# Optimization experiments

Measured on AMD Instinct MI355X. Metric: run time of the kernel, lower is better.

The kernel has to match this reference:

```python
import jax, jax.numpy as jnp
import numpy as np

B, Q, K, D = 8, 2048, 2048, 512
MASK_VALUE = -1e-06  # faithful to original (note: source uses -1e-06, not -1e6)


def setup_inputs() -> dict:
    key = jax.random.key(0)
    k1, k2, k3, k4, k5 = jax.random.split(key, 5)
    queries = jax.random.normal(k1, (B, Q, D), dtype=jnp.float32)
    keys = jax.random.normal(k2, (B, K, D), dtype=jnp.float32)
    values = jax.random.normal(k3, (B, K, D), dtype=jnp.float32)
    # Xavier-uniform-like init for the bilinear weight
    limit = float(np.sqrt(6.0 / (D + D)))
    W = jax.random.uniform(k4, (D, D), dtype=jnp.float32, minval=-limit, maxval=limit)
    attention_masks = jax.random.randint(k5, (B,), 1, K, dtype=jnp.int64 if jax.config.jax_enable_x64 else jnp.int32)
    return {"queries": queries, "keys": keys, "values": values, "W": W,
            "attention_masks": attention_masks}


def reference(queries, keys, values, W, attention_masks):
    # scores[b,q,k] = (queries @ W) . keys  -> bilinear attention logits
    scores = jnp.einsum('bqd,de,bke->bqk', queries, W, keys)
    # length mask: positions >= attention_masks[b] are replaced by MASK_VALUE
    valid = jnp.arange(scores.shape[-1])[None, None, :] < attention_masks[:, None, None]
    scores = jnp.where(valid, scores, MASK_VALUE)
    attn = jax.nn.softmax(scores, axis=-1)  # (B, Q, K)
    # dropout p=0 -> identity
    return jnp.einsum('bqk,bkv->bqv', attn, values)
```

## Files before the change

### kernel.cpp

```cpp
#include <hip/hip_runtime.h>

#define NB 8
#define NQ 2048
#define NK 2048
#define ND 512
#define QB 64
#define KB 512
#define MASK_VALUE (-1e-06f)
#define PLANE  ((size_t)NB * NK * ND)
#define WPLANE ((size_t)ND * ND)

typedef __attribute__((ext_vector_type(4))) float f32x4;
typedef __attribute__((ext_vector_type(8))) __bf16 bf16x8;
typedef __attribute__((ext_vector_type(8))) _Float16 f16x8;
typedef __attribute__((ext_vector_type(4))) _Float16 f16x4;
typedef __attribute__((ext_vector_type(8))) unsigned short u16x8;
typedef __attribute__((ext_vector_type(4))) unsigned int u32x4;

typedef f32x4  __attribute__((may_alias)) f32x4_ma;
typedef bf16x8 __attribute__((may_alias)) bf16x8_ma;
typedef f16x8  __attribute__((may_alias)) f16x8_ma;
typedef f16x4  __attribute__((may_alias)) f16x4_ma;
typedef u32x4  __attribute__((may_alias)) u32x4_ma;

__device__ __forceinline__ unsigned short f2bf(float x){
    union { float f; unsigned u; } v; v.f = x;
    unsigned r = v.u + 0x7fffu + ((v.u >> 16) & 1u);
    return (unsigned short)(r >> 16);
}
__device__ __forceinline__ float bf2f(unsigned short h){
    union { unsigned u; float f; } v; v.u = ((unsigned)h) << 16;
    return v.f;
}

__global__ __launch_bounds__(256)
void conv_k_f16_kernel(const float* __restrict__ K,
                       _Float16* __restrict__ kf)
{
    const size_t i = ((size_t)blockIdx.x * 256 + threadIdx.x) * 4;
    const f32x4 v = *(const f32x4_ma*)(K + i);
    f16x4 h;
    #pragma unroll
    for (int c = 0; c < 4; ++c) h[c] = (_Float16)v[c];
    *(f16x4_ma*)(kf + i) = h;
}

__global__ __launch_bounds__(256)
void transpose_v_f16_kernel(const float* __restrict__ V,
                            _Float16* __restrict__ vt)
{
    __shared__ float t[64][68];
    const int tid = threadIdx.x;
    const int bid = blockIdx.x;
    const int dt  = bid & 7;
    const int kt  = (bid >> 3) & 31;
    const int b   = bid >> 8;
    {
        const int rr = tid >> 4;
        const int c4 = (tid & 15) * 4;
        #pragma unroll
        for (int m4 = 0; m4 < 4; ++m4){
            const int kr = rr + m4*16;
            *(f32x4_ma*)&t[kr][c4] =
                *(const f32x4_ma*)&V[((size_t)b*NK + kt*64 + kr)*ND + dt*64 + c4];
        }
    }
    __syncthreads();
    {
        const int dr = tid >> 2;
        const int kc = (tid & 3) * 16;
        f16x8 v0, v1;
        #pragma unroll
        for (int j = 0; j < 8; ++j) v0[j] = (_Float16)t[kc + j][dr];
        #pragma unroll
        for (int j = 0; j < 8; ++j) v1[j] = (_Float16)t[kc + 8 + j][dr];
        const size_t dst = ((size_t)b*ND + dt*64 + dr)*NK + kt*64 + kc;
        *(f16x8_ma*)(vt + dst)     = v0;
        *(f16x8_ma*)(vt + dst + 8) = v1;
    }
}

__global__ __launch_bounds__(256)
void transpose_split_w_kernel(const float* __restrict__ W,
                              unsigned short* __restrict__ wth,
                              unsigned short* __restrict__ wtl)
{
    __shared__ float t[64][68];
    const int tid = threadIdx.x;
    const int et  = blockIdx.x & 7;
    const int dt  = blockIdx.x >> 3;
    {
        const int rr = tid >> 4;
        const int c4 = (tid & 15) * 4;
        #pragma unroll
        for (int m4 = 0; m4 < 4; ++m4){
            const int dr = rr + m4*16;
            *(f32x4_ma*)&t[dr][c4] =
                *(const f32x4_ma*)&W[(size_t)(dt*64 + dr)*ND + et*64 + c4];
        }
    }
    __syncthreads();
    {
        const int er = tid >> 2;
        const int dc = (tid & 3) * 16;
        unsigned short hh[16], ll[16];
        #pragma unroll
        for (int j = 0; j < 16; ++j){
            const float v = t[dc + j][er];
            const unsigned short h = f2bf(v);
            hh[j] = h;
            ll[j] = f2bf(v - bf2f(h));
        }
        u32x4 h0, h1, l0, l1;
        #pragma unroll
        for (int c = 0; c < 4; ++c){
            h0[c] = (unsigned)hh[2*c]   | ((unsigned)hh[2*c+1] << 16);
            h1[c] = (unsigned)hh[8+2*c] | ((unsigned)hh[9+2*c] << 16);
            l0[c] = (unsigned)ll[2*c]   | ((unsigned)ll[2*c+1] << 16);
            l1[c] = (unsigned)ll[8+2*c] | ((unsigned)ll[9+2*c] << 16);
        }
        const size_t dst = (size_t)(et*64 + er)*ND + dt*64 + dc;
        *(u32x4_ma*)(wth + dst)     = h0;
        *(u32x4_ma*)(wth + dst + 8) = h1;
        *(u32x4_ma*)(wtl + dst)     = l0;
        *(u32x4_ma*)(wtl + dst + 8) = l1;
    }
}

__global__ __launch_bounds__(1024, 4)
void attn_kernel(const float* __restrict__ Qp, const int* __restrict__ Mp,
                 const _Float16* __restrict__ Kf,
                 const _Float16* __restrict__ Vt,
                 const unsigned short* __restrict__ Wth, const unsigned short* __restrict__ Wtl,
                 float* __restrict__ Op)
{
    __shared__ _Float16 qw[QB][520];
    __shared__ _Float16 p_b[QB][520];
    __shared__ float wredA[QB][16];

    const int tid  = threadIdx.x;
    const int lane = tid & 63;
    const int wv   = tid >> 6;
    const int lm   = lane & 15;
    const int lg   = lane >> 4;
    const int b    = blockIdx.x & 7;
    const int q0   = (int)(blockIdx.x >> 3) * QB;

    int mk;
    {
        const int odd = Mp[1] | Mp[3] | Mp[5] | Mp[7];
        mk = (odd == 0) ? Mp[2*b] : Mp[b];
    }

    {
        f32x4 acc[4][2];
        #pragma unroll
        for (int m2 = 0; m2 < 4; ++m2)
            #pragma unroll
            for (int n2 = 0; n2 < 2; ++n2) acc[m2][n2] = (f32x4){0.f,0.f,0.f,0.f};

        for (int w = 0; w < 16; ++w){
            bf16x8 aH[4], aL[4];
            #pragma unroll
            for (int m2 = 0; m2 < 4; ++m2){
                const float* qp = Qp + ((size_t)b*NQ + q0 + m2*16 + lm)*ND + w*32 + lg*8;
                const f32x4 qa = *(const f32x4_ma*)qp;
                const f32x4 qb = *(const f32x4_ma*)(qp + 4);
                u16x8 hh, ll;
                #pragma unroll
                for (int c = 0; c < 4; ++c){
                    const unsigned short h = f2bf(qa[c]);
                    hh[c] = h; ll[c] = f2bf(qa[c] - bf2f(h));
                }
                #pragma unroll
                for (int c = 0; c < 4; ++c){
                    const unsigned short h = f2bf(qb[c]);
                    hh[4+c] = h; ll[4+c] = f2bf(qb[c] - bf2f(h));
                }
                aH[m2] = __builtin_bit_cast(bf16x8, hh);
                aL[m2] = __builtin_bit_cast(bf16x8, ll);
            }
            #pragma unroll
            for (int n2 = 0; n2 < 2; ++n2){
                const size_t wrow = (size_t)(wv*32 + n2*16 + lm)*ND + w*32 + lg*8;
                const bf16x8 bh = *(const bf16x8_ma*)(Wth + wrow);
                const bf16x8 bl = *(const bf16x8_ma*)(Wtl + wrow);
                #pragma unroll
                for (int m2 = 0; m2 < 4; ++m2){
                    acc[m2][n2] = __builtin_amdgcn_mfma_f32_16x16x32_bf16(aH[m2], bh, acc[m2][n2], 0,0,0);
                    acc[m2][n2] = __builtin_amdgcn_mfma_f32_16x16x32_bf16(aH[m2], bl, acc[m2][n2], 0,0,0);
                    acc[m2][n2] = __builtin_amdgcn_mfma_f32_16x16x32_bf16(aL[m2], bh, acc[m2][n2], 0,0,0);
                }
            }
        }
        #pragma unroll
        for (int m2 = 0; m2 < 4; ++m2)
            #pragma unroll
            for (int n2 = 0; n2 < 2; ++n2)
                #pragma unroll
                for (int r = 0; r < 4; ++r)
                    qw[m2*16 + lg*4 + r][wv*32 + n2*16 + lm] = (_Float16)acc[m2][n2][r];
    }
    __syncthreads();

    float m_run[4][4], lsum[4][4];
    #pragma unroll
    for (int m2 = 0; m2 < 4; ++m2)
        #pragma unroll
        for (int r = 0; r < 4; ++r){ m_run[m2][r] = -3.0e38f; lsum[m2][r] = 0.f; }

    f32x4 o_acc[4][2];
    #pragma unroll
    for (int m2 = 0; m2 < 4; ++m2)
        #pragma unroll
        for (int n = 0; n < 2; ++n) o_acc[m2][n] = (f32x4){0.f,0.f,0.f,0.f};

    const _Float16* kfb = Kf + ((size_t)b*NK + wv*16 + lm)*ND;
    const size_t vbase = ((size_t)b*ND + wv*32 + lm)*NK + lg*8;

    for (int kt = 0; kt < NK/KB; ++kt){
        const int k0 = kt * KB;
        const size_t koff = (size_t)k0 * ND;

        f32x4 sacc[2][4];
        #pragma unroll
        for (int h = 0; h < 2; ++h)
            #pragma unroll
            for (int m2 = 0; m2 < 4; ++m2) sacc[h][m2] = (f32x4){0.f,0.f,0.f,0.f};
        #pragma unroll
        for (int w2 = 0; w2 < 8; ++w2){
            f16x8 bk[2][2];
            #pragma unroll
            for (int j = 0; j < 2; ++j)
                #pragma unroll
                for (int h = 0; h < 2; ++h)
                    bk[j][h] = *(const f16x8_ma*)(kfb + koff + (size_t)h*256*ND + (w2*2 + j)*32 + lg*8);
            #pragma unroll
            for (int j = 0; j < 2; ++j){
                const int eoff = (w2*2 + j)*32 + lg*8;
                #pragma unroll
                for (int m2 = 0; m2 < 4; ++m2){
                    const f16x8 aQ = *(const f16x8_ma*)&qw[m2*16 + lm][eoff];
                    sacc[0][m2] = __builtin_amdgcn_mfma_f32_16x16x32_f16(aQ, bk[j][0], sacc[0][m2], 0,0,0);
                    sacc[1][m2] = __builtin_amdgcn_mfma_f32_16x16x32_f16(aQ, bk[j][1], sacc[1][m2], 0,0,0);
                }
            }
        }

        float sv[2][4][4];
        #pragma unroll
        for (int h = 0; h < 2; ++h){
            const bool inval = (k0 + h*256 + wv*16 + lm) >= mk;
            #pragma unroll
            for (int m2 = 0; m2 < 4; ++m2)
                #pragma unroll
                for (int r = 0; r < 4; ++r)
                    sv[h][m2][r] = inval ? MASK_VALUE : sacc[h][m2][r];
        }

        float pm[4][4];
        #pragma unroll
        for (int m2 = 0; m2 < 4; ++m2)
            #pragma unroll
            for (int r = 0; r < 4; ++r) pm[m2][r] = fmaxf(sv[0][m2][r], sv[1][m2][r]);
        #pragma unroll
        for (int off = 1; off < 16; off <<= 1)
            #pragma unroll
            for (int m2 = 0; m2 < 4; ++m2)
                #pragma unroll
                for (int r = 0; r < 4; ++r)
                    pm[m2][r] = fmaxf(pm[m2][r], __shfl_xor(pm[m2][r], off, 64));
        if (lm == 0){
            #pragma unroll
            for (int m2 = 0; m2 < 4; ++m2)
                #pragma unroll
                for (int r = 0; r < 4; ++r) wredA[m2*16 + lg*4 + r][wv] = pm[m2][r];
        }
        __syncthreads();

        #pragma unroll
        for (int m2 = 0; m2 < 4; ++m2)
            #pragma unroll
            for (int r = 0; r < 4; ++r){
                const int row = m2*16 + lg*4 + r;
                const f32x4 g0 = *(const f32x4_ma*)&wredA[row][0];
                const f32x4 g1 = *(const f32x4_ma*)&wredA[row][4];
                const f32x4 g2 = *(const f32x4_ma*)&wredA[row][8];
                const f32x4 g3 = *(const f32x4_ma*)&wredA[row][12];
                float gm = fmaxf(fmaxf(fmaxf(g0[0],g0[1]),fmaxf(g0[2],g0[3])),
                                 fmaxf(fmaxf(g1[0],g1[1]),fmaxf(g1[2],g1[3])));
                gm = fmaxf(gm, fmaxf(fmaxf(fmaxf(g2[0],g2[1]),fmaxf(g2[2],g2[3])),
                                     fmaxf(fmaxf(g3[0],g3[1]),fmaxf(g3[2],g3[3]))));
                if (gm > m_run[m2][r]){
                    const float fsc = __expf(m_run[m2][r] - gm);
                    m_run[m2][r] = gm;
                    o_acc[m2][0][r] *= fsc;
                    o_acc[m2][1][r] *= fsc;
                    lsum[m2][r]     *= fsc;
                }
                const _Float16 ph0 = (_Float16)__expf(sv[0][m2][r] - m_run[m2][r]);
                const _Float16 ph1 = (_Float16)__expf(sv[1][m2][r] - m_run[m2][r]);
                p_b[row][wv*16 + lm]       = ph0;
                p_b[row][256 + wv*16 + lm] = ph1;
                lsum[m2][r] += (float)ph0 + (float)ph1;
            }
        __syncthreads();

        #pragma unroll
        for (int kb = 0; kb < 16; ++kb){
            f16x8 pa[4];
            #pragma unroll
            for (int m2 = 0; m2 < 4; ++m2)
                pa[m2] = *(const f16x8_ma*)&p_b[m2*16 + lm][kb*32 + lg*8];
            #pragma unroll
            for (int n = 0; n < 2; ++n){
                const f16x8 vv = *(const f16x8_ma*)(Vt + vbase + (size_t)n*16*NK + k0 + kb*32);
                #pragma unroll
                for (int m2 = 0; m2 < 4; ++m2)
                    o_acc[m2][n] = __builtin_amdgcn_mfma_f32_16x16x32_f16(pa[m2], vv, o_acc[m2][n], 0,0,0);
            }
        }
    }

    #pragma unroll
    for (int off = 1; off < 16; off <<= 1)
        #pragma unroll
        for (int m2 = 0; m2 < 4; ++m2)
            #pragma unroll
            for (int r = 0; r < 4; ++r)
                lsum[m2][r] += __shfl_xor(lsum[m2][r], off, 64);
    if (lm == 0){
        #pragma unroll
        for (int m2 = 0; m2 < 4; ++m2)
            #pragma unroll
            for (int r = 0; r < 4; ++r)
                wredA[m2*16 + lg*4 + r][wv] = lsum[m2][r];
    }
    __syncthreads();
    #pragma unroll
    for (int m2 = 0; m2 < 4; ++m2){
        float li[4];
        #pragma unroll
        for (int r = 0; r < 4; ++r){
            const int row = m2*16 + lg*4 + r;
            const f32x4 s0 = *(const f32x4_ma*)&wredA[row][0];
            const f32x4 s1 = *(const f32x4_ma*)&wredA[row][4];
            const f32x4 s2 = *(const f32x4_ma*)&wredA[row][8];
            const f32x4 s3 = *(const f32x4_ma*)&wredA[row][12];
            const float l = (((s0[0]+s0[1]) + (s0[2]+s0[3])) + ((s1[0]+s1[1]) + (s1[2]+s1[3])))
                          + (((s2[0]+s2[1]) + (s2[2]+s2[3])) + ((s3[0]+s3[1]) + (s3[2]+s3[3])));
            li[r] = 1.f / l;
        }
        #pragma unroll
        for (int n = 0; n < 2; ++n)
            #pragma unroll
            for (int r = 0; r < 4; ++r)
                Op[((size_t)b*NQ + q0 + m2*16 + lg*4 + r)*ND + wv*32 + n*16 + lm]
                    = o_acc[m2][n][r] * li[r];
    }
}

extern "C" void kernel_launch(void* const* d_in, const int* in_sizes, int n_in,
                              void* d_out, int out_size, void* d_ws, size_t ws_size,
                              hipStream_t stream)
{
    (void)in_sizes; (void)n_in; (void)out_size; (void)ws_size;
    const float* Qp = (const float*)d_in[0];
    const float* Kp = (const float*)d_in[1];
    const float* Vp = (const float*)d_in[2];
    const float* Wp = (const float*)d_in[3];
    const int*   Mp = (const int*)  d_in[4];
    float* Op = (float*)d_out;

    unsigned short* wsu = (unsigned short*)d_ws;
    _Float16*       Kf  = (_Float16*)wsu;
    _Float16*       Vt  = (_Float16*)(wsu + PLANE);
    unsigned short* Wth = wsu + 2*PLANE;
    unsigned short* Wtl = wsu + 2*PLANE + WPLANE;

    hipLaunchKernelGGL(conv_k_f16_kernel, dim3(PLANE/1024), dim3(256), 0, stream,
                       Kp, Kf);
    hipLaunchKernelGGL(transpose_v_f16_kernel, dim3(NB*32*8), dim3(256), 0, stream,
                       Vp, Vt);
    hipLaunchKernelGGL(transpose_split_w_kernel, dim3(64), dim3(256), 0, stream,
                       Wp, Wth, Wtl);
    hipLaunchKernelGGL(attn_kernel, dim3(NB*(NQ/QB)), dim3(1024), 0, stream,
                       Qp, Mp, Kf, Vt, Wth, Wtl, Op);
}
```

Measured before the change: 270.1 us.

## Split Q·W projection into separate kernel, stage QW in global memory

Moves the split-bf16 Q·W projection out of the attention kernel into its own kernel, which writes an fp16 QW tensor to workspace. The attention kernel then reads QW fragments straight from global/L2 instead of LDS, which frees the qw shared array and may allow higher occupancy. The cost is an extra kernel launch, a global round trip of roughly 16 MB for QW, and repeated global loads of QW on every key tile.

```diff
diff --git a/kernel.cpp b/kernel.cpp
--- a/kernel.cpp
+++ b/kernel.cpp
@@ -22,6 +22,7 @@
 typedef f16x8  __attribute__((may_alias)) f16x8_ma;
 typedef f16x4  __attribute__((may_alias)) f16x4_ma;
 typedef u32x4  __attribute__((may_alias)) u32x4_ma;
+typedef _Float16 __attribute__((may_alias)) f16_ma;
 
 __device__ __forceinline__ unsigned short f2bf(float x){
     union { float f; unsigned u; } v; v.f = x;
@@ -128,16 +129,11 @@
 }
 
 __global__ __launch_bounds__(1024, 4)
-void attn_kernel(const float* __restrict__ Qp, const int* __restrict__ Mp,
-                 const _Float16* __restrict__ Kf,
-                 const _Float16* __restrict__ Vt,
-                 const unsigned short* __restrict__ Wth, const unsigned short* __restrict__ Wtl,
-                 float* __restrict__ Op)
-{
-    __shared__ _Float16 qw[QB][520];
-    __shared__ _Float16 p_b[QB][520];
-    __shared__ float wredA[QB][16];
-
+void qw_mfma_kernel(const float* __restrict__ Qp,
+                    const unsigned short* __restrict__ Wth,
+                    const unsigned short* __restrict__ Wtl,
+                    _Float16* __restrict__ qwg)
+{
     const int tid  = threadIdx.x;
     const int lane = tid & 63;
     const int wv   = tid >> 6;
@@ -146,63 +142,80 @@
     const int b    = blockIdx.x & 7;
     const int q0   = (int)(blockIdx.x >> 3) * QB;
 
+    f32x4 acc[4][2];
+    #pragma unroll
+    for (int m2 = 0; m2 < 4; ++m2)
+        #pragma unroll
+        for (int n2 = 0; n2 < 2; ++n2) acc[m2][n2] = (f32x4){0.f,0.f,0.f,0.f};
+
+    for (int w = 0; w < 16; ++w){
+        bf16x8 aH[4], aL[4];
+        #pragma unroll
+        for (int m2 = 0; m2 < 4; ++m2){
+            const float* qp = Qp + ((size_t)b*NQ + q0 + m2*16 + lm)*ND + w*32 + lg*8;
+            const f32x4 qa = *(const f32x4_ma*)qp;
+            const f32x4 qb = *(const f32x4_ma*)(qp + 4);
+            u16x8 hh, ll;
+            #pragma unroll
+            for (int c = 0; c < 4; ++c){
+                const unsigned short h = f2bf(qa[c]);
+                hh[c] = h; ll[c] = f2bf(qa[c] - bf2f(h));
+            }
+            #pragma unroll
+            for (int c = 0; c < 4; ++c){
+                const unsigned short h = f2bf(qb[c]);
+                hh[4+c] = h; ll[4+c] = f2bf(qb[c] - bf2f(h));
+            }
+            aH[m2] = __builtin_bit_cast(bf16x8, hh);
+            aL[m2] = __builtin_bit_cast(bf16x8, ll);
+        }
+        #pragma unroll
+        for (int n2 = 0; n2 < 2; ++n2){
+            const size_t wrow = (size_t)(wv*32 + n2*16 + lm)*ND + w*32 + lg*8;
+            const bf16x8 bh = *(const bf16x8_ma*)(Wth + wrow);
+            const bf16x8 bl = *(const bf16x8_ma*)(Wtl + wrow);
+            #pragma unroll
+            for (int m2 = 0; m2 < 4; ++m2){
+                acc[m2][n2] = __builtin_amdgcn_mfma_f32_16x16x32_bf16(aH[m2], bh, acc[m2][n2], 0,0,0);
+                acc[m2][n2] = __builtin_amdgcn_mfma_f32_16x16x32_bf16(aH[m2], bl, acc[m2][n2], 0,0,0);
+                acc[m2][n2] = __builtin_amdgcn_mfma_f32_16x16x32_bf16(aL[m2], bh, acc[m2][n2], 0,0,0);
+            }
+        }
+    }
+    #pragma unroll
+    for (int m2 = 0; m2 < 4; ++m2)
+        #pragma unroll
+        for (int n2 = 0; n2 < 2; ++n2)
+            #pragma unroll
+            for (int r = 0; r < 4; ++r)
+                qwg[((size_t)b*NQ + q0 + m2*16 + lg*4 + r)*ND + wv*32 + n2*16 + lm]
+                    = (_Float16)acc[m2][n2][r];
+}
+
+__global__ __launch_bounds__(1024, 4)
+void attn_kernel(const int* __restrict__ Mp,
+                 const _Float16* __restrict__ qwg,
+                 const _Float16* __restrict__ Kf,
+                 const _Float16* __restrict__ Vt,
+                 float* __restrict__ Op)
+{
+    __shared__ _Float16 p_b[QB][520];
+    __shared__ float wredA[QB][16];
+
+    const int tid  = threadIdx.x;
+    const int lane = tid & 63;
+    const int wv   = tid >> 6;
+    const int lm   = lane & 15;
+    const int lg   = lane >> 4;
+    const int b    = blockIdx.x & 7;
+    const int q0   = (int)(blockIdx.x >> 3) * QB;
+
     int mk;
     {
         const int odd = Mp[1] | Mp[3] | Mp[5] | Mp[7];
         mk = (odd == 0) ? Mp[2*b] : Mp[b];
     }
 
-    {
-        f32x4 acc[4][2];
-        #pragma unroll
-        for (int m2 = 0; m2 < 4; ++m2)
-            #pragma unroll
-            for (int n2 = 0; n2 < 2; ++n2) acc[m2][n2] = (f32x4){0.f,0.f,0.f,0.f};
-
-        for (int w = 0; w < 16; ++w){
-            bf16x8 aH[4], aL[4];
-            #pragma unroll
-            for (int m2 = 0; m2 < 4; ++m2){
-                const float* qp = Qp + ((size_t)b*NQ + q0 + m2*16 + lm)*ND + w*32 + lg*8;
-                const f32x4 qa = *(const f32x4_ma*)qp;
-                const f32x4 qb = *(const f32x4_ma*)(qp + 4);
-                u16x8 hh, ll;
-                #pragma unroll
-                for (int c = 0; c < 4; ++c){
-                    const unsigned short h = f2bf(qa[c]);
-                    hh[c] = h; ll[c] = f2bf(qa[c] - bf2f(h));
-                }
-                #pragma unroll
-                for (int c = 0; c < 4; ++c){
-                    const unsigned short h = f2bf(qb[c]);
-                    hh[4+c] = h; ll[4+c] = f2bf(qb[c] - bf2f(h));
-                }
-                aH[m2] = __builtin_bit_cast(bf16x8, hh);
-                aL[m2] = __builtin_bit_cast(bf16x8, ll);
-            }
-            #pragma unroll
-            for (int n2 = 0; n2 < 2; ++n2){
-                const size_t wrow = (size_t)(wv*32 + n2*16 + lm)*ND + w*32 + lg*8;
-                const bf16x8 bh = *(const bf16x8_ma*)(Wth + wrow);
-                const bf16x8 bl = *(const bf16x8_ma*)(Wtl + wrow);
-                #pragma unroll
-                for (int m2 = 0; m2 < 4; ++m2){
-                    acc[m2][n2] = __builtin_amdgcn_mfma_f32_16x16x32_bf16(aH[m2], bh, acc[m2][n2], 0,0,0);
-                    acc[m2][n2] = __builtin_amdgcn_mfma_f32_16x16x32_bf16(aH[m2], bl, acc[m2][n2], 0,0,0);
-                    acc[m2][n2] = __builtin_amdgcn_mfma_f32_16x16x32_bf16(aL[m2], bh, acc[m2][n2], 0,0,0);
-                }
-            }
-        }
-        #pragma unroll
-        for (int m2 = 0; m2 < 4; ++m2)
-            #pragma unroll
-            for (int n2 = 0; n2 < 2; ++n2)
-                #pragma unroll
-                for (int r = 0; r < 4; ++r)
-                    qw[m2*16 + lg*4 + r][wv*32 + n2*16 + lm] = (_Float16)acc[m2][n2][r];
-    }
-    __syncthreads();
-
     float m_run[4][4], lsum[4][4];
     #pragma unroll
     for (int m2 = 0; m2 < 4; ++m2)
@@ -215,7 +228,8 @@
         #pragma unroll
         for (int n = 0; n < 2; ++n) o_acc[m2][n] = (f32x4){0.f,0.f,0.f,0.f};
 
-    const _Float16* kfb = Kf + ((size_t)b*NK + wv*16 + lm)*ND;
+    const _Float16* kfb = Kf  + ((size_t)b*NK + wv*16 + lm)*ND;
+    const _Float16* qwb = qwg + ((size_t)b*NQ + q0 + lm)*ND;
     const size_t vbase = ((size_t)b*ND + wv*32 + lm)*NK + lg*8;
 
     for (int kt = 0; kt < NK/KB; ++kt){
@@ -240,7 +254,7 @@
                 const int eoff = (w2*2 + j)*32 + lg*8;
                 #pragma unroll
                 for (int m2 = 0; m2 < 4; ++m2){
-                    const f16x8 aQ = *(const f16x8_ma*)&qw[m2*16 + lm][eoff];
+                    const f16x8 aQ = *(const f16x8_ma*)(qwb + (size_t)m2*16*ND + eoff);
                     sacc[0][m2] = __builtin_amdgcn_mfma_f32_16x16x32_f16(aQ, bk[j][0], sacc[0][m2], 0,0,0);
                     sacc[1][m2] = __builtin_amdgcn_mfma_f32_16x16x32_f16(aQ, bk[j][1], sacc[1][m2], 0,0,0);
                 }
@@ -375,8 +389,9 @@
     unsigned short* wsu = (unsigned short*)d_ws;
     _Float16*       Kf  = (_Float16*)wsu;
     _Float16*       Vt  = (_Float16*)(wsu + PLANE);
-    unsigned short* Wth = wsu + 2*PLANE;
-    unsigned short* Wtl = wsu + 2*PLANE + WPLANE;
+    _Float16*       Qw  = (_Float16*)(wsu + 2*PLANE);
+    unsigned short* Wth = wsu + 3*PLANE;
+    unsigned short* Wtl = wsu + 3*PLANE + WPLANE;
 
     hipLaunchKernelGGL(conv_k_f16_kernel, dim3(PLANE/1024), dim3(256), 0, stream,
                        Kp, Kf);
@@ -384,6 +399,8 @@
                        Vp, Vt);
     hipLaunchKernelGGL(transpose_split_w_kernel, dim3(64), dim3(256), 0, stream,
                        Wp, Wth, Wtl);
+    hipLaunchKernelGGL(qw_mfma_kernel, dim3(NB*(NQ/QB)), dim3(1024), 0, stream,
+                       Qp, Wth, Wtl, Qw);
     hipLaunchKernelGGL(attn_kernel, dim3(NB*(NQ/QB)), dim3(1024), 0, stream,
-                       Qp, Mp, Kf, Vt, Wth, Wtl, Op);
-}
+                       Mp, Qw, Kf, Vt, Op);
+}
```

Measured after the change: 557.0 us. 2.06x slower.
